# Performance work log

Hardware: AMD Instinct MI355X
Metric: run time of the kernel (lower is better)

The kernel has to match this reference:

```python
import jax, jax.numpy as jnp
import numpy as np

BATCH, SEQ, DIM = 4, 2048, 1024
HEADS = 16
HD = DIM // HEADS  # 64
BASE = 10000.0


def setup_inputs() -> dict:
    key = jax.random.key(0)
    k1, k2, k3 = jax.random.split(key, 3)
    x = jax.random.normal(k1, (BATCH, SEQ, DIM), dtype=jnp.float32)
    # torch Linear weight is (out,in); we store transposed (in,out) so y = x @ w
    w_qkv = jax.random.normal(k2, (DIM, 3 * DIM), dtype=jnp.float32) * (DIM ** -0.5)
    w_out = jax.random.normal(k3, (DIM, DIM), dtype=jnp.float32) * (DIM ** -0.5)
    return {"x": x, "w_qkv": w_qkv, "w_out": w_out}


def _rope_cos_sin(seq_len: int, head_dim: int):
    inv_freq = 1.0 / (BASE ** (jnp.arange(0, head_dim, 2, dtype=jnp.float32) / head_dim))
    t = jnp.arange(seq_len, dtype=jnp.float32)
    freqs = t[:, None] * inv_freq[None, :]          # (S, HD/2)
    emb = jnp.concatenate([freqs, freqs], axis=-1)  # (S, HD)
    return jnp.cos(emb), jnp.sin(emb)


def _rotate_half(x):
    x1, x2 = jnp.split(x, 2, axis=-1)
    return jnp.concatenate([-x2, x1], axis=-1)


def reference(x, w_qkv, w_out):
    B, S, D = x.shape
    qkv = x @ w_qkv                                  # (B,S,3D)
    q, k, v = jnp.split(qkv, 3, axis=-1)
    # (B,S,D) -> (B,H,S,HD)
    q = q.reshape(B, S, HEADS, HD).transpose(0, 2, 1, 3)
    k = k.reshape(B, S, HEADS, HD).transpose(0, 2, 1, 3)
    v = v.reshape(B, S, HEADS, HD).transpose(0, 2, 1, 3)
    cos, sin = _rope_cos_sin(S, HD)                  # (S,HD), broadcast over B,H
    q = q * cos + _rotate_half(q) * sin
    k = k * cos + _rotate_half(k) * sin
    scale = HD ** -0.5
    scores = jnp.einsum('bhqd,bhkd->bhqk', q, k) * scale  # (B,H,S,S)
    causal = jnp.tril(jnp.ones((S, S), dtype=bool))
    scores = jnp.where(causal, scores, -jnp.inf)
    attn = jax.nn.softmax(scores, axis=-1)
    out = jnp.einsum('bhqk,bhkd->bhqd', attn, v)     # (B,H,S,HD)
    out = out.transpose(0, 2, 1, 3).reshape(B, S, D)
    out = out @ w_out
    return out, k, v
```

## Files before the change

### kernel.cpp

```cpp
#include <hip/hip_runtime.h>
#include <hip/hip_bf16.h>
#include <stdint.h>

#define BATCH 4
#define SEQ 2048
#define DIM 1024
#define HEADS 16
#define HD 64
#define BH (BATCH*HEADS)
#define NQKV (3*DIM)

typedef __attribute__((ext_vector_type(8))) short bf16x8;
typedef __attribute__((ext_vector_type(4))) float f32x4;
typedef __attribute__((ext_vector_type(16))) float f32x16;
typedef __attribute__((ext_vector_type(4))) unsigned u32x4;

#define MFMA16(a,b,c) __builtin_amdgcn_mfma_f32_16x16x32_bf16(a,b,c,0,0,0)
#define MFMA32(a,b,c) __builtin_amdgcn_mfma_f32_32x32x16_bf16(a,b,c,0,0,0)

#if __has_builtin(__builtin_amdgcn_exp2f)
#define EXP2(x) __builtin_amdgcn_exp2f(x)
#else
#define EXP2(x) exp2f(x)
#endif

__device__ inline float bf2f(short s){
    unsigned u = ((unsigned)(unsigned short)s) << 16;
    float f;
    __builtin_memcpy(&f, &u, 4);
    return f;
}
__device__ inline unsigned cvt_pk_bf16(float lo, float hi){
    unsigned r;
    asm("v_cvt_pk_bf16_f32 %0, %1, %2" : "=v"(r) : "v"(lo), "v"(hi));
    return r;
}
__device__ inline short cv1(float f){
    return (short)(cvt_pk_bf16(f, f) & 0xffffu);
}

__global__ void conv_bf16(const float* __restrict__ in, short* __restrict__ out, int n4){
    int i = blockIdx.x*blockDim.x + threadIdx.x;
    f32x4 v = *(const f32x4*)&in[(size_t)i*4];
    unsigned lo = cvt_pk_bf16(v[0], v[1]);
    unsigned hi = cvt_pk_bf16(v[2], v[3]);
    unsigned out2[2] = {lo, hi};
    __builtin_memcpy(&out[(size_t)i*4], out2, 8);
}

__global__ void transpose_conv(const float* __restrict__ in, short* __restrict__ out, int R, int C){
    __shared__ float tile[32][33];
    int c0 = blockIdx.x*32, r0 = blockIdx.y*32;
    int tx = threadIdx.x, ty = threadIdx.y;
    #pragma unroll
    for (int dy = 0; dy < 32; dy += 8)
        tile[ty+dy][tx] = in[(size_t)(r0+ty+dy)*C + c0+tx];
    __syncthreads();
    #pragma unroll
    for (int dy = 0; dy < 32; dy += 8)
        out[(size_t)(c0+ty+dy)*R + r0+tx] = cv1(tile[tx][ty+dy]);
}

__global__ __launch_bounds__(512) void gemm_bt2(const short* __restrict__ A, const short* __restrict__ Bt,
                        short* __restrict__ Cout, int M, int N, int K)
{
    __shared__ short As[2][8192];
    __shared__ short Bs[2][4096];
    const int t = threadIdx.x;
    const int lane = t & 63, wave = t >> 6;
    const int wr = wave >> 1, wc = wave & 1;
    const int nbn = N >> 7;
    const int cpx = gridDim.x >> 3;
    const int swz = (blockIdx.x & 7) * cpx + (blockIdx.x >> 3);
    const int bm = swz / nbn, bn = swz % nbn;
    const int m0 = bm*256, n0 = bn*128;
    const int l15 = lane & 15, lhi = lane >> 4;

    f32x4 acc[4][4];
    #pragma unroll
    for (int i=0;i<4;i++)
        #pragma unroll
        for (int j=0;j<4;j++) acc[i][j] = (f32x4){0.f,0.f,0.f,0.f};

    for (int k0 = 0; k0 < K; k0 += 64) {
        #pragma unroll
        for (int kk = 0; kk < 2; ++kk) {
            #pragma unroll
            for (int it = 0; it < 2; ++it) {
                int base = (it*512 + wave*64)*8;
                int off  = base + lane*8;
                int row = off >> 5, col = off & 31;
                __builtin_amdgcn_global_load_lds(
                    (const __attribute__((address_space(1))) void*)(A + (size_t)(m0+row)*K + k0 + kk*32 + col),
                    (__attribute__((address_space(3))) void*)(&As[kk][base]), 16, 0, 0);
            }
            {
                int base = (wave*64)*8;
                int off  = base + lane*8;
                int row = off >> 5, col = off & 31;
                __builtin_amdgcn_global_load_lds(
                    (const __attribute__((address_space(1))) void*)(Bt + (size_t)(n0+row)*K + k0 + kk*32 + col),
                    (__attribute__((address_space(3))) void*)(&Bs[kk][base]), 16, 0, 0);
            }
        }
        __syncthreads();
        #pragma unroll
        for (int kk = 0; kk < 2; ++kk) {
            bf16x8 a[4], b[4];
            #pragma unroll
            for (int i=0;i<4;i++)
                a[i] = *(const bf16x8*)&As[kk][(wr*64 + i*16 + l15)*32 + lhi*8];
            #pragma unroll
            for (int j=0;j<4;j++)
                b[j] = *(const bf16x8*)&Bs[kk][(wc*64 + j*16 + l15)*32 + lhi*8];
            #pragma unroll
            for (int i=0;i<4;i++)
                #pragma unroll
                for (int j=0;j<4;j++)
                    acc[i][j] = MFMA16(a[i], b[j], acc[i][j]);
        }
        __syncthreads();
    }

    #pragma unroll
    for (int i=0;i<4;i++)
        #pragma unroll
        for (int j=0;j<4;j++)
            #pragma unroll
            for (int jj=0;jj<4;jj++) {
                int row = m0 + wr*64 + i*16 + lhi*4 + jj;
                int col = n0 + wc*64 + j*16 + l15;
                Cout[(size_t)row*N + col] = cv1(acc[i][j][jj]);
            }
}

__global__ __launch_bounds__(256) void gemm_out(const short* __restrict__ obuf,
        const float* __restrict__ lbuf, const short* __restrict__ Bt,
        float* __restrict__ Cout)
{
    const int N = 1024, K = 1024;
    __shared__ short As[2*128*32];
    __shared__ short Bs[2*128*32];
    const int t = threadIdx.x;
    const int lane = t & 63, wave = t >> 6;
    const int wr = wave >> 1, wc = wave & 1;
    const int nbn = 8;
    const int cpx = gridDim.x >> 3;
    const int swz = (blockIdx.x & 7) * cpx + (blockIdx.x >> 3);
    const int bm = swz / nbn, bn = swz % nbn;
    const int m0 = bm*128, n0 = bn*128;
    const int l15 = lane & 15, lhi = lane >> 4;

    f32x4 acc[4][4];
    #pragma unroll
    for (int i=0;i<4;i++)
        #pragma unroll
        for (int j=0;j<4;j++) acc[i][j] = (f32x4){0.f,0.f,0.f,0.f};

    for (int k0 = 0; k0 < K; k0 += 64) {
        #pragma unroll
        for (int kk = 0; kk < 2; ++kk) {
            #pragma unroll
            for (int it = 0; it < 2; ++it) {
                const int loff = (it*256 + wave*64 + lane)*8;
                const int row = loff >> 5, col = loff & 31;
                const int grow = m0 + row;
                const int gcol = k0 + kk*32 + col;
                const int bq = grow >> 11, q = grow & 2047;
                const int h = gcol >> 6, d = gcol & 63;
                const size_t tile = ((size_t)(bq*16 + h) << 6) + (q >> 5);
                const short* op = obuf + tile*4096 + (q & 31)*64 + d;
                bf16x8 a0 = *(const bf16x8*)op;
                bf16x8 a1 = *(const bf16x8*)(op + 2048);
                const float* lb = lbuf + tile*64 + (q & 31);
                float inv = 1.0f / (lb[0] + lb[32]);
                unsigned w[4];
                #pragma unroll
                for (int j=0;j<4;j++)
                    w[j] = cvt_pk_bf16((bf2f(a0[2*j])   + bf2f(a1[2*j]))   * inv,
                                       (bf2f(a0[2*j+1]) + bf2f(a1[2*j+1])) * inv);
                __builtin_memcpy(&As[kk*4096 + loff], w, 16);

                const int base = kk*4096 + (it*256 + wave*64)*8;
                __builtin_amdgcn_global_load_lds(
                    (const __attribute__((address_space(1))) void*)(Bt + (size_t)(n0+row)*K + gcol),
                    (__attribute__((address_space(3))) void*)(Bs + base), 16, 0, 0);
            }
        }
        __syncthreads();
        #pragma unroll
        for (int kk = 0; kk < 2; ++kk) {
            bf16x8 a[4], b[4];
            #pragma unroll
            for (int i=0;i<4;i++)
                a[i] = *(const bf16x8*)&As[kk*4096 + (wr*64 + i*16 + l15)*32 + lhi*8];
            #pragma unroll
            for (int j=0;j<4;j++)
                b[j] = *(const bf16x8*)&Bs[kk*4096 + (wc*64 + j*16 + l15)*32 + lhi*8];
            #pragma unroll
            for (int i=0;i<4;i++)
                #pragma unroll
                for (int j=0;j<4;j++)
                    acc[i][j] = MFMA16(a[i], b[j], acc[i][j]);
        }
        __syncthreads();
    }

    #pragma unroll
    for (int i=0;i<4;i++)
        #pragma unroll
        for (int j=0;j<4;j++)
            #pragma unroll
            for (int jj=0;jj<4;jj++) {
                int row = m0 + wr*64 + i*16 + lhi*4 + jj;
                int col = n0 + wc*64 + j*16 + l15;
                Cout[(size_t)row*N + col] = acc[i][j][jj];
            }
}

__global__ __launch_bounds__(256) void rope_scatter(const short* __restrict__ qkvb,
                             short* __restrict__ qp, short* __restrict__ kp,
                             short* __restrict__ vp,
                             float* __restrict__ kout, float* __restrict__ vout)
{
    __shared__ short vt[64*72];
    const int t = threadIdx.x;
    const int bh = blockIdx.x >> 5;
    const int sb = blockIdx.x & 31;
    const int b = bh >> 4, h = bh & 15;
    const int s_loc = t >> 2, ic = (t & 3) << 3;
    const int s = (sb << 6) + s_loc;
    const size_t rowbase = ((size_t)(b*SEQ + s))*NQKV + h*HD;

    bf16x8 q1 = *(const bf16x8*)&qkvb[rowbase + ic];
    bf16x8 q2 = *(const bf16x8*)&qkvb[rowbase + ic + 32];
    bf16x8 k1 = *(const bf16x8*)&qkvb[rowbase + DIM + ic];
    bf16x8 k2 = *(const bf16x8*)&qkvb[rowbase + DIM + ic + 32];
    bf16x8 v1 = *(const bf16x8*)&qkvb[rowbase + 2*DIM + ic];
    bf16x8 v2 = *(const bf16x8*)&qkvb[rowbase + 2*DIM + ic + 32];

    const float QS = 0.125f * 1.4426950408889634f;
    float q1s[8], q2s[8], k1f[8], k2f[8], v1f[8], v2f[8];
    #pragma unroll
    for (int j=0;j<8;j++){
        int i = ic + j;
        float inv = exp2f(-(float)i * (13.287712379549449f/32.0f));
        float ang = (float)s * inv;
        float sn, cs;
        sincosf(ang, &sn, &cs);
        float q1f = bf2f(q1[j]), q2f = bf2f(q2[j]);
        float ka = bf2f(k1[j]), kb_ = bf2f(k2[j]);
        float qr1 = q1f*cs - q2f*sn, qr2 = q2f*cs + q1f*sn;
        float kr1 = ka*cs - kb_*sn,  kr2 = kb_*cs + ka*sn;
        q1s[j] = qr1*QS; q2s[j] = qr2*QS;
        k1f[j] = kr1; k2f[j] = kr2;
        v1f[j] = bf2f(v1[j]); v2f[j] = bf2f(v2[j]);
    }
    bf16x8 qo1, qo2, ko1, ko2;
    {
        unsigned w[4];
        #pragma unroll
        for (int j=0;j<4;j++) w[j] = cvt_pk_bf16(q1s[2*j], q1s[2*j+1]);
        __builtin_memcpy(&qo1, w, 16);
        #pragma unroll
        for (int j=0;j<4;j++) w[j] = cvt_pk_bf16(q2s[2*j], q2s[2*j+1]);
        __builtin_memcpy(&qo2, w, 16);
        #pragma unroll
        for (int j=0;j<4;j++) w[j] = cvt_pk_bf16(k1f[2*j], k1f[2*j+1]);
        __builtin_memcpy(&ko1, w, 16);
        #pragma unroll
        for (int j=0;j<4;j++) w[j] = cvt_pk_bf16(k2f[2*j], k2f[2*j+1]);
        __builtin_memcpy(&ko2, w, 16);
    }

    const size_t obase = ((size_t)bh*SEQ + s)*HD;
    #pragma unroll
    for (int j4=0;j4<2;j4++){
        *(f32x4*)&kout[obase+ic+j4*4]    = (f32x4){k1f[j4*4],k1f[j4*4+1],k1f[j4*4+2],k1f[j4*4+3]};
        *(f32x4*)&kout[obase+ic+32+j4*4] = (f32x4){k2f[j4*4],k2f[j4*4+1],k2f[j4*4+2],k2f[j4*4+3]};
        *(f32x4*)&vout[obase+ic+j4*4]    = (f32x4){v1f[j4*4],v1f[j4*4+1],v1f[j4*4+2],v1f[j4*4+3]};
        *(f32x4*)&vout[obase+ic+32+j4*4] = (f32x4){v2f[j4*4],v2f[j4*4+1],v2f[j4*4+2],v2f[j4*4+3]};
    }

    {
        const int tkv = (sb << 1) + (s_loc >> 5);
        const int rlo = s_loc & 31;
        const int g1 = ic >> 3,   i1 = g1 >> 1, H1 = g1 & 1;
        const int g2 = 4+(ic>>3), i2 = g2 >> 1, H2 = g2 & 1;
        const size_t tb = ((size_t)bh*64 + tkv)*4;
        *(bf16x8*)&qp[(tb + i1)*512 + (H1*32 + rlo)*8] = qo1;
        *(bf16x8*)&qp[(tb + i2)*512 + (H2*32 + rlo)*8] = qo2;
        *(bf16x8*)&kp[(tb + i1)*512 + (H1*32 + rlo)*8] = ko1;
        *(bf16x8*)&kp[(tb + i2)*512 + (H2*32 + rlo)*8] = ko2;
    }

    #pragma unroll
    for (int j=0;j<8;j++){
        int i = ic + j;
        vt[i*72 + ((((s_loc>>3) ^ (i&7) ^ (i>>3)) & 7)<<3) + (s_loc&7)] = v1[j];
        int i2 = i + 32;
        vt[i2*72 + ((((s_loc>>3) ^ (i2&7) ^ (i2>>3)) & 7)<<3) + (s_loc&7)] = v2[j];
    }
    __syncthreads();

    const int i_out = t >> 2, g = t & 3;
    const int nn = i_out >> 5, l31v = i_out & 31;
    #pragma unroll
    for (int cc=0; cc<2; ++cc){
        int c = 2*g + cc;
        bf16x8 rv = *(const bf16x8*)&vt[i_out*72 + ((((c) ^ (i_out&7) ^ (i_out>>3)) & 7)<<3)];
        int tkv = (sb << 1) + (c >> 2);
        int m = (c >> 1) & 1, H = c & 1;
        size_t va = ((((size_t)bh*64 + tkv)*2 + nn)*2 + m)*512 + (H*32 + l31v)*8;
        *(bf16x8*)&vp[va] = rv;
    }
}

#define ATT_BODY(KU, KP) do { \
    const unsigned sOff = (unsigned)step << 11; \
    { int npos = step + 1; npos = (npos < hi) ? npos : step; \
      const unsigned pOff = (unsigned)npos << 11; \
      _Pragma("unroll") \
      for (int i=0;i<4;i++) \
          KP[i] = *(const bf16x8*)&kbase[pOff + i*512 + lane*8]; } \
    bf16x8 vf[2][2]; \
    _Pragma("unroll") \
    for (int nn=0;nn<2;nn++) \
        _Pragma("unroll") \
        for (int m=0;m<2;m++) \
            vf[nn][m] = *(const bf16x8*)&vbase[sOff + nn*1024 + m*512 + lane*8]; \
    __builtin_amdgcn_s_setprio(1); \
    f32x16 sacc; \
    _Pragma("unroll") \
    for (int rr=0;rr<16;rr++) sacc[rr] = 0.f; \
    _Pragma("unroll") \
    for (int i=0;i<4;i++) \
        sacc = MFMA32(KU[i], qf[i], sacc); \
    __builtin_amdgcn_s_setprio(0); \
    if (step == n-1) { \
        const int kv0 = step << 5; \
        _Pragma("unroll") \
        for (int rr=0;rr<16;rr++){ \
            int kv = kv0 + (rr&3) + 8*(rr>>2) + 4*H; \
            if (kv > q0 + l31) sacc[rr] = -3.0e38f; \
        } \
    } \
    float p[16]; \
    _Pragma("unroll") \
    for (int rr=0;rr<16;rr++) p[rr] = EXP2(sacc[rr]); \
    unsigned W0 = cvt_pk_bf16(p[0],  p[1]); \
    unsigned W1 = cvt_pk_bf16(p[2],  p[3]); \
    unsigned W2 = cvt_pk_bf16(p[4],  p[5]); \
    unsigned W3 = cvt_pk_bf16(p[6],  p[7]); \
    unsigned W4 = cvt_pk_bf16(p[8],  p[9]); \
    unsigned W5 = cvt_pk_bf16(p[10], p[11]); \
    unsigned W6 = cvt_pk_bf16(p[12], p[13]); \
    unsigned W7 = cvt_pk_bf16(p[14], p[15]); \
    asm("v_permlane32_swap_b32 %0, %1" : "+v"(W0), "+v"(W2)); \
    asm("v_permlane32_swap_b32 %0, %1" : "+v"(W1), "+v"(W3)); \
    asm("v_permlane32_swap_b32 %0, %1" : "+v"(W4), "+v"(W6)); \
    asm("v_permlane32_swap_b32 %0, %1" : "+v"(W5), "+v"(W7)); \
    u32x4 paw0 = (u32x4){W0, W1, W2, W3}; \
    u32x4 paw1 = (u32x4){W4, W5, W6, W7}; \
    bf16x8 pa[2]; \
    __builtin_memcpy(&pa[0], &paw0, 16); \
    __builtin_memcpy(&pa[1], &paw1, 16); \
    __builtin_amdgcn_s_setprio(1); \
    _Pragma("unroll") \
    for (int nn=0;nn<2;nn++) \
        _Pragma("unroll") \
        for (int m=0;m<2;m++) \
            o[nn] = MFMA32(pa[m], vf[nn][m], o[nn]); \
    psum = MFMA32(pa[0], onesf, psum); \
    psum = MFMA32(pa[1], onesf, psum); \
    __builtin_amdgcn_s_setprio(0); \
} while(0)

__global__ __launch_bounds__(64) void attn_partial(
        const short* __restrict__ qp, const short* __restrict__ kp,
        const short* __restrict__ vp, short* __restrict__ obuf,
        float* __restrict__ lbuf)
{
    const int lane = threadIdx.x;
    const int wg = blockIdx.x;
    const int x = wg & 7;
    const int r = wg >> 3;
    const int half = r & 1;
    const int pp = (r >> 1) & 31;
    const int bh = (x << 3) | (r >> 6);
    const int l31 = lane & 31;
    const int H = lane >> 5;
    const short* kbase = kp + (size_t)bh * 64 * 2048;
    const short* vbase = vp + (size_t)bh * 64 * 2048;
    const short* qbase = qp + (size_t)bh * 64 * 2048;

    bf16x8 onesf;
    #pragma unroll
    for (int j=0;j<8;j++) onesf[j] = (short)0x3F80;

    #pragma unroll 1
    for (int part = 0; part < 2; ++part) {
        const int qt = part ? (63 - pp) : pp;
        const int q0 = qt << 5;
        const int n  = qt + 1;
        const int mid = (n + 1) >> 1;
        const int lo = half ? mid : 0;
        const int hi = half ? n : mid;

        bf16x8 qf[4];
        #pragma unroll
        for (int i=0;i<4;i++)
            qf[i] = *(const bf16x8*)&qbase[(unsigned)qt*2048 + i*512 + lane*8];

        f32x16 o[2], psum;
        #pragma unroll
        for (int nn=0;nn<2;nn++)
            #pragma unroll
            for (int rr=0;rr<16;rr++) o[nn][rr] = 0.f;
        #pragma unroll
        for (int rr=0;rr<16;rr++) psum[rr] = 0.f;

        if (lo < hi) {
            bf16x8 kfA[4], kfB[4];
            #pragma unroll
            for (int i=0;i<4;i++)
                kfA[i] = *(const bf16x8*)&kbase[(unsigned)lo*2048 + i*512 + lane*8];

            int step = lo;
            while (1) {
                ATT_BODY(kfA, kfB);
                ++step; if (step >= hi) break;
                ATT_BODY(kfB, kfA);
                ++step; if (step >= hi) break;
            }
        }

        short* ob = obuf + (size_t)(((bh << 6) | qt)*2 + half) * 2048;
        #pragma unroll
        for (int nn=0;nn<2;nn++)
            #pragma unroll
            for (int rr=0;rr<16;rr++){
                int qloc = (rr&3) + 8*(rr>>2) + 4*H;
                ob[qloc*64 + nn*32 + l31] = cv1(o[nn][rr]);
            }
        float* lb = lbuf + (size_t)(((bh << 6) | qt)*2 + half) * 32;
        if (l31 == 0) {
            #pragma unroll
            for (int rr=0;rr<16;rr++){
                int qloc = (rr&3) + 8*(rr>>2) + 4*H;
                lb[qloc] = psum[rr];
            }
        }
    }
}
#undef ATT_BODY

extern "C" void kernel_launch(void* const* d_in, const int* in_sizes, int n_in,
                              void* d_out, int out_size, void* d_ws, size_t ws_size,
                              hipStream_t stream) {
    const float* x     = (const float*)d_in[0];
    const float* w_qkv = (const float*)d_in[1];
    const float* w_out = (const float*)d_in[2];
    float* out  = (float*)d_out;
    float* kout = out + (size_t)BATCH*SEQ*DIM;
    float* vout = kout + (size_t)BH*SEQ*HD;

    char* ws = (char*)d_ws;
    short* xb    = (short*)(ws + 0);
    short* wqkvT = (short*)(ws + 16777216);
    short* woutT = (short*)(ws + 23068672);
    short* qkvb  = (short*)(ws + 25165824);
    short* obuf  = (short*)(ws + 25165824);
    float* lbuf  = (float*)(ws + 25165824 + 33554432);
    short* qp    = (short*)(ws + 75497472);
    short* kp    = (short*)(ws + 92274688);
    short* vp    = (short*)(ws + 109051904);

    conv_bf16<<<(BATCH*SEQ*DIM)/1024, 256, 0, stream>>>(x, xb, (BATCH*SEQ*DIM)/4);
    transpose_conv<<<dim3(NQKV/32, DIM/32), dim3(32,8), 0, stream>>>(w_qkv, wqkvT, DIM, NQKV);
    transpose_conv<<<dim3(DIM/32, DIM/32), dim3(32,8), 0, stream>>>(w_out, woutT, DIM, DIM);

    gemm_bt2<<<(8192/256)*(NQKV/128), 512, 0, stream>>>(xb, wqkvT, qkvb, 8192, NQKV, DIM);

    rope_scatter<<<BH*(SEQ/64), 256, 0, stream>>>(qkvb, qp, kp, vp, kout, vout);

    attn_partial<<<4096, 64, 0, stream>>>(qp, kp, vp, obuf, lbuf);

    gemm_out<<<(8192/128)*(DIM/128), 256, 0, stream>>>(obuf, lbuf, woutT, out);
}
```

Baseline: 205.6 us.

## Double-buffer QKV GEMM K-tiles with async global-to-LDS prefetch

The QKV projection GEMM previously loaded two 32-wide K chunks, synchronized, computed on both, then synchronized again, so global loads never overlapped with MFMA work. It now stages one 32-wide K chunk at a time into alternating LDS buffers, issuing the next chunk's global_load_lds before computing on the current one and using explicit vmcnt/lgkmcnt waits with raw s_barrier. It also raises wave priority around the MFMA block. The cost is twice as many barriers per unit of K work and a reliance on hand-placed waitcnt counts being correct.

```diff
diff --git a/kernel.cpp b/kernel.cpp
--- a/kernel.cpp
+++ b/kernel.cpp
@@ -76,51 +76,63 @@
     const int m0 = bm*256, n0 = bn*128;
     const int l15 = lane & 15, lhi = lane >> 4;
 
+    const int baseA0 = (wave*64)*8,        offA0 = baseA0 + lane*8;
+    const int baseA1 = (512 + wave*64)*8,  offA1 = baseA1 + lane*8;
+    const int rowA0 = offA0 >> 5, colA0 = offA0 & 31;
+    const int rowA1 = offA1 >> 5, colA1 = offA1 & 31;
+    const int baseB = (wave*64)*8,         offB = baseB + lane*8;
+    const int rowB = offB >> 5, colB = offB & 31;
+
+#define STAGE2(buf, kc) do { \
+    __builtin_amdgcn_global_load_lds( \
+        (const __attribute__((address_space(1))) void*)(A + (size_t)(m0+rowA0)*K + (kc) + colA0), \
+        (__attribute__((address_space(3))) void*)(&As[buf][baseA0]), 16, 0, 0); \
+    __builtin_amdgcn_global_load_lds( \
+        (const __attribute__((address_space(1))) void*)(A + (size_t)(m0+rowA1)*K + (kc) + colA1), \
+        (__attribute__((address_space(3))) void*)(&As[buf][baseA1]), 16, 0, 0); \
+    __builtin_amdgcn_global_load_lds( \
+        (const __attribute__((address_space(1))) void*)(Bt + (size_t)(n0+rowB)*K + (kc) + colB), \
+        (__attribute__((address_space(3))) void*)(&Bs[buf][baseB]), 16, 0, 0); \
+} while(0)
+
     f32x4 acc[4][4];
     #pragma unroll
     for (int i=0;i<4;i++)
         #pragma unroll
         for (int j=0;j<4;j++) acc[i][j] = (f32x4){0.f,0.f,0.f,0.f};
 
-    for (int k0 = 0; k0 < K; k0 += 64) {
-        #pragma unroll
-        for (int kk = 0; kk < 2; ++kk) {
-            #pragma unroll
-            for (int it = 0; it < 2; ++it) {
-                int base = (it*512 + wave*64)*8;
-                int off  = base + lane*8;
-                int row = off >> 5, col = off & 31;
-                __builtin_amdgcn_global_load_lds(
-                    (const __attribute__((address_space(1))) void*)(A + (size_t)(m0+row)*K + k0 + kk*32 + col),
-                    (__attribute__((address_space(3))) void*)(&As[kk][base]), 16, 0, 0);
-            }
-            {
-                int base = (wave*64)*8;
-                int off  = base + lane*8;
-                int row = off >> 5, col = off & 31;
-                __builtin_amdgcn_global_load_lds(
-                    (const __attribute__((address_space(1))) void*)(Bt + (size_t)(n0+row)*K + k0 + kk*32 + col),
-                    (__attribute__((address_space(3))) void*)(&Bs[kk][base]), 16, 0, 0);
-            }
+    STAGE2(0, 0);
+    const int nt = K >> 5;
+    for (int ti = 0; ti < nt; ++ti) {
+        const int cur = ti & 1;
+        if (ti + 1 < nt) {
+            STAGE2(cur^1, (ti+1) << 5);
+            asm volatile("s_waitcnt vmcnt(3)" ::: "memory");
+        } else {
+            asm volatile("s_waitcnt vmcnt(0)" ::: "memory");
         }
-        __syncthreads();
-        #pragma unroll
-        for (int kk = 0; kk < 2; ++kk) {
-            bf16x8 a[4], b[4];
-            #pragma unroll
-            for (int i=0;i<4;i++)
-                a[i] = *(const bf16x8*)&As[kk][(wr*64 + i*16 + l15)*32 + lhi*8];
+        __builtin_amdgcn_s_barrier();
+        __builtin_amdgcn_sched_barrier(0);
+
+        bf16x8 a[4], b[4];
+        #pragma unroll
+        for (int i=0;i<4;i++)
+            a[i] = *(const bf16x8*)&As[cur][(wr*64 + i*16 + l15)*32 + lhi*8];
+        #pragma unroll
+        for (int j=0;j<4;j++)
+            b[j] = *(const bf16x8*)&Bs[cur][(wc*64 + j*16 + l15)*32 + lhi*8];
+        __builtin_amdgcn_s_setprio(1);
+        #pragma unroll
+        for (int i=0;i<4;i++)
             #pragma unroll
             for (int j=0;j<4;j++)
-                b[j] = *(const bf16x8*)&Bs[kk][(wc*64 + j*16 + l15)*32 + lhi*8];
-            #pragma unroll
-            for (int i=0;i<4;i++)
-                #pragma unroll
-                for (int j=0;j<4;j++)
-                    acc[i][j] = MFMA16(a[i], b[j], acc[i][j]);
-        }
-        __syncthreads();
-    }
+                acc[i][j] = MFMA16(a[i], b[j], acc[i][j]);
+        __builtin_amdgcn_s_setprio(0);
+
+        asm volatile("s_waitcnt lgkmcnt(0)" ::: "memory");
+        __builtin_amdgcn_s_barrier();
+    }
+#undef STAGE2
 
     #pragma unroll
     for (int i=0;i<4;i++)
```

After: 208.0 us. Within noise of the previous version (+1.2%).
